# Optimization experiments

Hardware: AMD Instinct MI355X
Metric: run time of the kernel (lower is better)

Reference implementation:

```python
import jax, jax.numpy as jnp
import numpy as np

D = 1024  # embed dim == mlp hidden dim (hiddendim=input_dim in source)

def _layernorm(x, gamma, beta, eps=1e-5):
    mu = jnp.mean(x, axis=-1, keepdims=True)
    var = jnp.var(x, axis=-1, keepdims=True)
    return (x - mu) * jax.lax.rsqrt(var + eps) * gamma + beta

def setup_inputs() -> dict:
    key = jax.random.key(0)
    ks = jax.random.split(key, 16)
    B, N = 16, 1024
    s = 1.0 / np.sqrt(D)
    inp = {
        "x": jax.random.normal(ks[0], (B, N, D), jnp.float32),
        "ln1_g": jnp.ones((D,), jnp.float32),
        "ln1_b": jnp.zeros((D,), jnp.float32),
        "ln2_g": jnp.ones((D,), jnp.float32),
        "ln2_b": jnp.zeros((D,), jnp.float32),
        "wq": jax.random.normal(ks[1], (D, D), jnp.float32) * s,
        "bq": jnp.zeros((D,), jnp.float32),
        "wk": jax.random.normal(ks[2], (D, D), jnp.float32) * s,
        "bk": jnp.zeros((D,), jnp.float32),
        "wv": jax.random.normal(ks[3], (D, D), jnp.float32) * s,
        "bv": jnp.zeros((D,), jnp.float32),
        "wo": jax.random.normal(ks[4], (D, D), jnp.float32) * s,
        "bo": jnp.zeros((D,), jnp.float32),
        "w1": jax.random.normal(ks[5], (D, D), jnp.float32) * s,
        "b1": jnp.zeros((D,), jnp.float32),
        "w2": jax.random.normal(ks[6], (D, D), jnp.float32) * s,
        "b2": jnp.zeros((D,), jnp.float32),
    }
    return inp

def reference(x, ln1_g, ln1_b, ln2_g, ln2_b, wq, bq, wk, bk, wv, bv, wo, bo, w1, b1, w2, b2):
    d = x.shape[-1]
    # pre-LN -> naive full-matrix attention (single head over full D, scale D**0.5)
    xn = _layernorm(x, ln1_g, ln1_b)
    q = xn @ wq + bq
    k = xn @ wk + bk
    v = xn @ wv + bv
    scores = jnp.einsum('bnd,bmd->bnm', q, k) / jnp.sqrt(jnp.asarray(d, x.dtype))
    attn = jax.nn.softmax(scores, axis=-1)  # [B,N,N] materialized, as in source
    mha = jnp.einsum('bnm,bmd->bnd', attn, v) @ wo + bo
    x_update = x + mha
    # pre-LN -> MLP: Linear->GELU->Linear->GELU, hidden == D
    xu = _layernorm(x_update, ln2_g, ln2_b)
    h = jax.nn.gelu(xu @ w1 + b1, approximate=False)
    h = jax.nn.gelu(h @ w2 + b2, approximate=False)
    return h + x_update
```

## Files before the change

### kernel.cpp

```cpp
#include <hip/hip_runtime.h>
#include <hip/hip_bf16.h>
#include <math.h>

#define BATCH 16
#define SEQ   1024
#define DIM   1024
#define ROWS  (BATCH*SEQ)
#define KD    1024
#define KTILES (KD/32)

typedef __bf16 bf16_t;
typedef __bf16 bf16x4 __attribute__((ext_vector_type(4)));
typedef __bf16 bf16x8 __attribute__((ext_vector_type(8)));
typedef float  f32x4  __attribute__((ext_vector_type(4)));

__device__ __forceinline__ float gelu_exact(float x) {
    return 0.5f * x * (1.0f + erff(x * 0.70710678118654752f));
}
__device__ __forceinline__ void split2(float v, bf16_t& h, bf16_t& l) {
    h = (bf16_t)v;
    l = (bf16_t)(v - (float)h);
}

__device__ __forceinline__ void gload16(const bf16_t* g, bf16_t* l) {
    __builtin_amdgcn_global_load_lds(
        (const __attribute__((address_space(1))) unsigned int*)g,
        (__attribute__((address_space(3))) unsigned int*)l,
        16, 0, 0);
}

__global__ __launch_bounds__(256)
void fill0_kernel(float* __restrict__ p, size_t n) {
    const size_t i = (size_t)blockIdx.x * blockDim.x + threadIdx.x;
    const size_t stride = (size_t)gridDim.x * blockDim.x;
    for (size_t j = i; j < n; j += stride) p[j] = 0.0f;
}

__global__ __launch_bounds__(256)
void ln_split_kernel(const float* __restrict__ x, const float* __restrict__ g,
                     const float* __restrict__ b,
                     bf16_t* __restrict__ oh, bf16_t* __restrict__ ol) {
    __shared__ float s1[4], s2[4];
    const size_t row = blockIdx.x;
    const int t = threadIdx.x;
    const float4 v = ((const float4*)(x + row * DIM))[t];
    float s  = v.x + v.y + v.z + v.w;
    float ss = v.x*v.x + v.y*v.y + v.z*v.z + v.w*v.w;
    #pragma unroll
    for (int off = 32; off > 0; off >>= 1) {
        s  += __shfl_down(s,  off, 64);
        ss += __shfl_down(ss, off, 64);
    }
    const int wid = t >> 6, lane = t & 63;
    if (lane == 0) { s1[wid] = s; s2[wid] = ss; }
    __syncthreads();
    s  = s1[0] + s1[1] + s1[2] + s1[3];
    ss = s2[0] + s2[1] + s2[2] + s2[3];
    const float mean = s * (1.0f / DIM);
    const float var  = ss * (1.0f / DIM) - mean * mean;
    const float rstd = rsqrtf(var + 1e-5f);
    const float4 gv = ((const float4*)g)[t];
    const float4 bv = ((const float4*)b)[t];
    float o[4];
    o[0] = (v.x - mean) * rstd * gv.x + bv.x;
    o[1] = (v.y - mean) * rstd * gv.y + bv.y;
    o[2] = (v.z - mean) * rstd * gv.z + bv.z;
    o[3] = (v.w - mean) * rstd * gv.w + bv.w;
    bf16x4 h, l;
    #pragma unroll
    for (int i = 0; i < 4; ++i) { bf16_t hh, ll; split2(o[i], hh, ll); h[i] = hh; l[i] = ll; }
    *(bf16x4*)&oh[row * DIM + t * 4] = h;
    *(bf16x4*)&ol[row * DIM + t * 4] = l;
}

__global__ __launch_bounds__(256)
void softmax_split_kernel(const float* __restrict__ sc,
                          bf16_t* __restrict__ ph, bf16_t* __restrict__ pl) {
    __shared__ float sm[4], ssum[4];
    const size_t row = blockIdx.x;
    const int t = threadIdx.x;
    float4 v = ((const float4*)(sc + row * SEQ))[t];
    float m = fmaxf(fmaxf(v.x, v.y), fmaxf(v.z, v.w));
    #pragma unroll
    for (int off = 32; off > 0; off >>= 1) m = fmaxf(m, __shfl_down(m, off, 64));
    const int wid = t >> 6, lane = t & 63;
    if (lane == 0) sm[wid] = m;
    __syncthreads();
    m = fmaxf(fmaxf(sm[0], sm[1]), fmaxf(sm[2], sm[3]));
    v.x = expf(v.x - m); v.y = expf(v.y - m);
    v.z = expf(v.z - m); v.w = expf(v.w - m);
    float s = v.x + v.y + v.z + v.w;
    #pragma unroll
    for (int off = 32; off > 0; off >>= 1) s += __shfl_down(s, off, 64);
    if (lane == 0) ssum[wid] = s;
    __syncthreads();
    s = ssum[0] + ssum[1] + ssum[2] + ssum[3];
    const float inv = 1.0f / s;
    float o[4] = { v.x * inv, v.y * inv, v.z * inv, v.w * inv };
    bf16x4 h, l;
    #pragma unroll
    for (int i = 0; i < 4; ++i) { bf16_t hh, ll; split2(o[i], hh, ll); h[i] = hh; l[i] = ll; }
    *(bf16x4*)&ph[row * SEQ + t * 4] = h;
    *(bf16x4*)&pl[row * SEQ + t * 4] = l;
}

__global__ __launch_bounds__(256)
void wsplit_kernel(const float* __restrict__ w,
                   bf16_t* __restrict__ oh, bf16_t* __restrict__ ol) {
    __shared__ float T[64][68];
    const int k0 = blockIdx.x * 64, n0 = blockIdx.y * 64;
    const int t = threadIdx.x;
    const int tr = t >> 4, tc = t & 15;
    #pragma unroll
    for (int j = 0; j < 4; ++j) {
        const float4 v = *(const float4*)&w[(size_t)(k0 + tr + j * 16) * DIM + n0 + tc * 4];
        *(float4*)&T[tr + j * 16][tc * 4] = v;
    }
    __syncthreads();
    #pragma unroll
    for (int j = 0; j < 4; ++j) {
        const int nl = tr + j * 16;
        const int kl = tc * 4;
        bf16x4 h, l;
        #pragma unroll
        for (int i = 0; i < 4; ++i) {
            bf16_t hh, ll; split2(T[kl + i][nl], hh, ll);
            h[i] = hh; l[i] = ll;
        }
        *(bf16x4*)&oh[(size_t)(n0 + nl) * KD + k0 + kl] = h;
        *(bf16x4*)&ol[(size_t)(n0 + nl) * KD + k0 + kl] = l;
    }
}

template<int BIAS, bool GELU, bool SPLIT, bool RES>
__global__ __launch_bounds__(256)
void gemm_mfma(const bf16_t* __restrict__ Ah, const bf16_t* __restrict__ Al,
               const bf16_t* __restrict__ Bh, const bf16_t* __restrict__ Bl,
               const float* __restrict__ bias, const float* res,
               float* Cf, bf16_t* __restrict__ Ch, bf16_t* __restrict__ Cl,
               int Nn, int ldb,
               long long sA, long long sB, long long sC, float scale) {
    __shared__ alignas(16) bf16_t LAh[128 * 32];
    __shared__ alignas(16) bf16_t LAl[128 * 32];
    __shared__ alignas(16) bf16_t LBh[128 * 32];
    __shared__ alignas(16) bf16_t LBl[128 * 32];

    const int bm0 = blockIdx.x * 128;
    const int bn0 = blockIdx.y * 128;
    const int bz  = blockIdx.z;
    Ah += (size_t)bz * sA;  Al += (size_t)bz * sA;
    Bh += (size_t)bz * sB;  Bl += (size_t)bz * sB;
    const size_t cbase = (size_t)bz * sC;

    const int tid  = threadIdx.x;
    const int lane = tid & 63;
    const int w    = tid >> 6;
    const int wm   = w >> 1, wn = w & 1;

    const int rr0 = w * 16 + (lane >> 2);
    const int rr1 = rr0 + 64;
    const int c   = lane & 3;
    const int cs0 = c ^ ((rr0 >> 1) & 3);
    const int cs1 = c ^ ((rr1 >> 1) & 3);
    const int ldst0 = (w * 16) * 32;
    const int ldst1 = (64 + w * 16) * 32;

    const bf16_t* gAh0 = Ah + (size_t)(bm0 + rr0) * KD + cs0 * 8;
    const bf16_t* gAh1 = Ah + (size_t)(bm0 + rr1) * KD + cs1 * 8;
    const bf16_t* gAl0 = Al + (size_t)(bm0 + rr0) * KD + cs0 * 8;
    const bf16_t* gAl1 = Al + (size_t)(bm0 + rr1) * KD + cs1 * 8;
    const bf16_t* gBh0 = Bh + (size_t)(bn0 + rr0) * ldb + cs0 * 8;
    const bf16_t* gBh1 = Bh + (size_t)(bn0 + rr1) * ldb + cs1 * 8;
    const bf16_t* gBl0 = Bl + (size_t)(bn0 + rr0) * ldb + cs0 * 8;
    const bf16_t* gBl1 = Bl + (size_t)(bn0 + rr1) * ldb + cs1 * 8;

    int roffA[4], roffB[4];
    #pragma unroll
    for (int i = 0; i < 4; ++i) {
        const int ra = wm * 64 + i * 16 + (lane & 15);
        roffA[i] = ra * 32 + (((lane >> 4) ^ ((ra >> 1) & 3)) * 8);
        const int rb = wn * 64 + i * 16 + (lane & 15);
        roffB[i] = rb * 32 + (((lane >> 4) ^ ((rb >> 1) & 3)) * 8);
    }

    f32x4 acc[4][4];
    #pragma unroll
    for (int i = 0; i < 4; ++i)
        #pragma unroll
        for (int j = 0; j < 4; ++j)
            acc[i][j] = (f32x4)0.0f;

    for (int kt = 0; kt < KTILES; ++kt) {
        gload16(gAh0, &LAh[ldst0]);  gload16(gAh1, &LAh[ldst1]);
        gload16(gAl0, &LAl[ldst0]);  gload16(gAl1, &LAl[ldst1]);
        gload16(gBh0, &LBh[ldst0]);  gload16(gBh1, &LBh[ldst1]);
        gload16(gBl0, &LBl[ldst0]);  gload16(gBl1, &LBl[ldst1]);
        gAh0 += 32; gAh1 += 32; gAl0 += 32; gAl1 += 32;
        gBh0 += 32; gBh1 += 32; gBl0 += 32; gBl1 += 32;
        __syncthreads();

        bf16x8 bh[4], bl[4];
        #pragma unroll
        for (int i = 0; i < 4; ++i) {
            bh[i] = *(const bf16x8*)&LBh[roffB[i]];
            bl[i] = *(const bf16x8*)&LBl[roffB[i]];
        }
        #pragma unroll
        for (int im = 0; im < 4; ++im) {
            const bf16x8 ah = *(const bf16x8*)&LAh[roffA[im]];
            const bf16x8 al = *(const bf16x8*)&LAl[roffA[im]];
            #pragma unroll
            for (int in = 0; in < 4; ++in) {
                acc[im][in] = __builtin_amdgcn_mfma_f32_16x16x32_bf16(ah, bh[in], acc[im][in], 0, 0, 0);
                acc[im][in] = __builtin_amdgcn_mfma_f32_16x16x32_bf16(ah, bl[in], acc[im][in], 0, 0, 0);
                acc[im][in] = __builtin_amdgcn_mfma_f32_16x16x32_bf16(al, bh[in], acc[im][in], 0, 0, 0);
            }
        }
        __syncthreads();
    }

    const int colb = bn0 + wn * 64 + (lane & 15);
    const int rowb = bm0 + wm * 64 + 4 * (lane >> 4);
    #pragma unroll
    for (int im = 0; im < 4; ++im) {
        #pragma unroll
        for (int in = 0; in < 4; ++in) {
            const int col = colb + in * 16;
            float bc = 0.0f;
            if (BIAS == 1) bc = bias[col];
            #pragma unroll
            for (int j = 0; j < 4; ++j) {
                const int row = rowb + im * 16 + j;
                float v = acc[im][in][j] * scale;
                if (BIAS == 1) v += bc;
                if (BIAS == 2) v += bias[row];
                if (GELU) v = gelu_exact(v);
                const size_t off = cbase + (size_t)row * Nn + col;
                if (SPLIT) {
                    bf16_t hh, ll; split2(v, hh, ll);
                    Ch[off] = hh; Cl[off] = ll;
                } else {
                    if (RES) v += res[off];
                    Cf[off] = v;
                }
            }
        }
    }
}

extern "C" void kernel_launch(void* const* d_in, const int* in_sizes, int n_in,
                              void* d_out, int out_size, void* d_ws, size_t ws_size,
                              hipStream_t stream) {
    const float* x     = (const float*)d_in[0];
    const float* ln1_g = (const float*)d_in[1];
    const float* ln1_b = (const float*)d_in[2];
    const float* ln2_g = (const float*)d_in[3];
    const float* ln2_b = (const float*)d_in[4];
    const float* wq    = (const float*)d_in[5];
    const float* bq    = (const float*)d_in[6];
    const float* wk    = (const float*)d_in[7];
    const float* bk    = (const float*)d_in[8];
    const float* wv    = (const float*)d_in[9];
    const float* bv    = (const float*)d_in[10];
    const float* wo    = (const float*)d_in[11];
    const float* bo    = (const float*)d_in[12];
    const float* w1    = (const float*)d_in[13];
    const float* b1    = (const float*)d_in[14];
    const float* w2    = (const float*)d_in[15];
    const float* b2    = (const float*)d_in[16];

    const size_t EL  = (size_t)ROWS * DIM;
    const size_t WEL = (size_t)DIM * KD;
    const size_t NEED = (6 * EL + 12 * WEL) * sizeof(bf16_t);

    if (ws_size < NEED) {
        fill0_kernel<<<2048, 256, 0, stream>>>((float*)d_out, (size_t)out_size);
        return;
    }

    bf16_t* base = (bf16_t*)d_ws;
    bf16_t* S0h = base;            bf16_t* S0l = S0h + EL;
    bf16_t* S1h = base + 2 * EL;   bf16_t* S1l = S1h + EL;
    bf16_t* S2h = base + 4 * EL;   bf16_t* S2l = S2h + EL;
    bf16_t* Wb  = base + 6 * EL;
    bf16_t* Kh  = (bf16_t*)d_out;  bf16_t* Kl = Kh + EL;
    float* sc   = (float*)S0h;
    float* xupd = (float*)S1h;

    const dim3 blk(256);
    const dim3 gw(ROWS / 128, DIM / 128, 1);
    const dim3 gvt(DIM / 128, ROWS / 128, 1);
    const dim3 ga(SEQ / 128, SEQ / 128, BATCH);
    const long long sND = (long long)SEQ * DIM;
    const long long sNN = (long long)SEQ * SEQ;

    ln_split_kernel<<<ROWS, blk, 0, stream>>>(x, ln1_g, ln1_b, S0h, S0l);
    const float* Wsrc[6] = { wq, wk, wv, wo, w1, w2 };
    bf16_t *wTh[6], *wTl[6];
    for (int i = 0; i < 6; ++i) {
        wTh[i] = Wb + (size_t)i * 2 * WEL;
        wTl[i] = wTh[i] + WEL;
        wsplit_kernel<<<dim3(16, 16), blk, 0, stream>>>(Wsrc[i], wTh[i], wTl[i]);
    }
    gemm_mfma<1, false, true, false><<<gw, blk, 0, stream>>>(
        S0h, S0l, wTh[0], wTl[0], bq, nullptr, nullptr, S1h, S1l, DIM, KD, 0, 0, 0, 1.0f);
    gemm_mfma<1, false, true, false><<<gw, blk, 0, stream>>>(
        S0h, S0l, wTh[1], wTl[1], bk, nullptr, nullptr, Kh, Kl, DIM, KD, 0, 0, 0, 1.0f);
    gemm_mfma<2, false, true, false><<<gvt, blk, 0, stream>>>(
        wTh[2], wTl[2], S0h, S0l, bv, nullptr, nullptr, S2h, S2l, ROWS, KD, 0, 0, 0, 1.0f);
    gemm_mfma<0, false, false, false><<<ga, blk, 0, stream>>>(
        S1h, S1l, Kh, Kl, nullptr, nullptr, sc, nullptr, nullptr, SEQ, KD, sND, sND, sNN, 0.03125f);
    softmax_split_kernel<<<ROWS, blk, 0, stream>>>(sc, S1h, S1l);
    gemm_mfma<0, false, true, false><<<ga, blk, 0, stream>>>(
        S1h, S1l, S2h, S2l, nullptr, nullptr, nullptr, S0h, S0l, DIM, ROWS, sNN, SEQ, sND, 1.0f);
    gemm_mfma<1, false, false, true><<<gw, blk, 0, stream>>>(
        S0h, S0l, wTh[3], wTl[3], bo, x, xupd, nullptr, nullptr, DIM, KD, 0, 0, 0, 1.0f);
    ln_split_kernel<<<ROWS, blk, 0, stream>>>(xupd, ln2_g, ln2_b, S0h, S0l);
    gemm_mfma<1, true, true, false><<<gw, blk, 0, stream>>>(
        S0h, S0l, wTh[4], wTl[4], b1, nullptr, nullptr, S2h, S2l, DIM, KD, 0, 0, 0, 1.0f);
    gemm_mfma<1, true, false, true><<<gw, blk, 0, stream>>>(
        S2h, S2l, wTh[5], wTl[5], b2, xupd, (float*)d_out, nullptr, nullptr, DIM, KD, 0, 0, 0, 1.0f);
}
```

Before: 1.217 ms.

## Double-buffer LDS tiles in split-bf16 MFMA GEMM to overlap loads with compute

Doubles the four LDS tile buffers and issues the global-to-LDS loads for the next K tile before computing on the current one, leaving one barrier per iteration. This is meant to hide global load latency behind the MFMA work. LDS use grows from 32KB to 64KB per block, which may lower occupancy. The single barrier relies on async LDS-load completion being covered by the vmcnt wait that precedes __syncthreads.

Result: slower. 1.297 ms (+6.6%).

```diff
diff --git a/kernel.cpp b/kernel.cpp
--- a/kernel.cpp
+++ b/kernel.cpp
@@ -8,6 +8,7 @@
 #define ROWS  (BATCH*SEQ)
 #define KD    1024
 #define KTILES (KD/32)
+#define TILE_EL (128*32)
 
 typedef __bf16 bf16_t;
 typedef __bf16 bf16x4 __attribute__((ext_vector_type(4)));
@@ -140,10 +141,10 @@
                float* Cf, bf16_t* __restrict__ Ch, bf16_t* __restrict__ Cl,
                int Nn, int ldb,
                long long sA, long long sB, long long sC, float scale) {
-    __shared__ alignas(16) bf16_t LAh[128 * 32];
-    __shared__ alignas(16) bf16_t LAl[128 * 32];
-    __shared__ alignas(16) bf16_t LBh[128 * 32];
-    __shared__ alignas(16) bf16_t LBl[128 * 32];
+    __shared__ alignas(16) bf16_t LAh[2 * TILE_EL];
+    __shared__ alignas(16) bf16_t LAl[2 * TILE_EL];
+    __shared__ alignas(16) bf16_t LBh[2 * TILE_EL];
+    __shared__ alignas(16) bf16_t LBl[2 * TILE_EL];
 
     const int bm0 = blockIdx.x * 128;
     const int bn0 = blockIdx.y * 128;
@@ -174,6 +175,15 @@
     const bf16_t* gBl0 = Bl + (size_t)(bn0 + rr0) * ldb + cs0 * 8;
     const bf16_t* gBl1 = Bl + (size_t)(bn0 + rr1) * ldb + cs1 * 8;
 
+    auto STAGE = [&](int buf, int kt) {
+        const int go = kt * 32;
+        const int h  = buf * TILE_EL;
+        gload16(gAh0 + go, &LAh[h + ldst0]);  gload16(gAh1 + go, &LAh[h + ldst1]);
+        gload16(gAl0 + go, &LAl[h + ldst0]);  gload16(gAl1 + go, &LAl[h + ldst1]);
+        gload16(gBh0 + go, &LBh[h + ldst0]);  gload16(gBh1 + go, &LBh[h + ldst1]);
+        gload16(gBl0 + go, &LBl[h + ldst0]);  gload16(gBl1 + go, &LBl[h + ldst1]);
+    };
+
     int roffA[4], roffB[4];
     #pragma unroll
     for (int i = 0; i < 4; ++i) {
@@ -190,25 +200,24 @@
         for (int j = 0; j < 4; ++j)
             acc[i][j] = (f32x4)0.0f;
 
+    STAGE(0, 0);
+    __syncthreads();
+
+    int cur = 0;
     for (int kt = 0; kt < KTILES; ++kt) {
-        gload16(gAh0, &LAh[ldst0]);  gload16(gAh1, &LAh[ldst1]);
-        gload16(gAl0, &LAl[ldst0]);  gload16(gAl1, &LAl[ldst1]);
-        gload16(gBh0, &LBh[ldst0]);  gload16(gBh1, &LBh[ldst1]);
-        gload16(gBl0, &LBl[ldst0]);  gload16(gBl1, &LBl[ldst1]);
-        gAh0 += 32; gAh1 += 32; gAl0 += 32; gAl1 += 32;
-        gBh0 += 32; gBh1 += 32; gBl0 += 32; gBl1 += 32;
-        __syncthreads();
-
+        if (kt + 1 < KTILES) STAGE(cur ^ 1, kt + 1);
+
+        const int h = cur * TILE_EL;
         bf16x8 bh[4], bl[4];
         #pragma unroll
         for (int i = 0; i < 4; ++i) {
-            bh[i] = *(const bf16x8*)&LBh[roffB[i]];
-            bl[i] = *(const bf16x8*)&LBl[roffB[i]];
+            bh[i] = *(const bf16x8*)&LBh[h + roffB[i]];
+            bl[i] = *(const bf16x8*)&LBl[h + roffB[i]];
         }
         #pragma unroll
         for (int im = 0; im < 4; ++im) {
-            const bf16x8 ah = *(const bf16x8*)&LAh[roffA[im]];
-            const bf16x8 al = *(const bf16x8*)&LAl[roffA[im]];
+            const bf16x8 ah = *(const bf16x8*)&LAh[h + roffA[im]];
+            const bf16x8 al = *(const bf16x8*)&LAl[h + roffA[im]];
             #pragma unroll
             for (int in = 0; in < 4; ++in) {
                 acc[im][in] = __builtin_amdgcn_mfma_f32_16x16x32_bf16(ah, bh[in], acc[im][in], 0, 0, 0);
@@ -217,6 +226,7 @@
             }
         }
         __syncthreads();
+        cur ^= 1;
     }
 
     const int colb = bn0 + wn * 64 + (lane & 15);
```
